# Optimization experiments

Measured on AMD Instinct MI355X. Metric: run time of the kernel, lower is better.

The kernel has to match this reference:

```python
import jax, jax.numpy as jnp
import numpy as np
from jax import lax

TEMPERATURE = 34.0
PAD = 1

def setup_inputs() -> dict:
    key = jax.random.key(0)
    ks = jax.random.split(key, 6)
    B, C, H, W = 16, 256, 64, 64
    K, O, kk, hidden = 4, 256, 3, int(256 * 0.25) + 1
    return {
        "x": jax.random.normal(ks[0], (B, C, H, W), jnp.float32),
        "w_fc1": jax.random.normal(ks[1], (hidden, C), jnp.float32) * 0.05,
        "w_fc2": jax.random.normal(ks[2], (K, hidden), jnp.float32) * 0.05,
        "b_fc2": jax.random.normal(ks[3], (K,), jnp.float32) * 0.05,
        "weight": jax.random.normal(ks[4], (K, O, C, kk, kk), jnp.float32) * 0.05,
        "bias": jax.random.normal(ks[5], (K, O), jnp.float32) * 0.05,
    }

def reference(x, w_fc1, w_fc2, b_fc2, weight, bias):
    # attention2d: global avg pool -> 1x1 conv -> relu -> 1x1 conv -> softmax(logits/T)
    pooled = jnp.mean(x, axis=(2, 3))                       # [B, C]
    h = jax.nn.relu(pooled @ w_fc1.T)                       # [B, hidden]
    logits = h @ w_fc2.T + b_fc2                            # [B, K]
    att = jax.nn.softmax(logits / TEMPERATURE, axis=1)      # [B, K]

    K = weight.shape[0]
    # per-sample aggregated kernels/bias
    agg_w = jnp.einsum('bk,koihw->boihw', att, weight)      # [B, O, C, k, k]
    agg_b = att @ bias                                      # [B, O]

    def conv_one(xi, wi):
        # xi: [C, H, W], wi: [O, C, k, k]
        return lax.conv_general_dilated(
            xi[None], wi, window_strides=(1, 1),
            padding=[(PAD, PAD), (PAD, PAD)],
            dimension_numbers=('NCHW', 'OIHW', 'NCHW'))[0]

    out = jax.vmap(conv_one)(x, agg_w)                      # [B, O, H, W]
    return out + agg_b[:, :, None, None]
```

## Files before the change

### kernel.cpp

```cpp
#include <hip/hip_runtime.h>
#include <math.h>

constexpr int B   = 16;
constexpr int C   = 256;
constexpr int H   = 64;
constexpr int W   = 64;
constexpr int K   = 4;
constexpr int O   = 256;
constexpr int HID = 65;
constexpr float TEMP = 34.0f;

typedef __bf16 bf16x8 __attribute__((ext_vector_type(8)));
typedef float  f32x16 __attribute__((ext_vector_type(16)));
typedef unsigned short ushort_t;

__device__ inline ushort_t f2bf(float f) {
    union { float f; unsigned u; } v; v.f = f;
    unsigned u = v.u;
    u += 0x7FFF + ((u >> 16) & 1);
    return (ushort_t)(u >> 16);
}

__device__ inline void gl2lds16(const void* g, void* l) {
    __builtin_amdgcn_global_load_lds(
        (const __attribute__((address_space(1))) unsigned int*)g,
        (__attribute__((address_space(3))) unsigned int*)l, 16, 0, 0);
}

__global__ void tp_kernel(const float* __restrict__ x,
                          ushort_t* __restrict__ xT,
                          float* __restrict__ pooled) {
    const int ci = blockIdx.x, yg = blockIdx.y, b = blockIdx.z;
    const int tid = threadIdx.x;
    const int cc = tid >> 4;
    const int yy = tid & 15;
    const int y  = yg * 16 + yy;
    const int c  = ci * 16 + cc;

    __shared__ ushort_t t_lds[16 * 1040];
    __shared__ float pool_l[16];
    if (tid < 16) pool_l[tid] = 0.f;
    __syncthreads();

    const float4* src = (const float4*)(x + (((size_t)b * C + c) * H + y) * W);
    float s = 0.f;
    #pragma unroll
    for (int i = 0; i < 16; ++i) {
        float4 v = src[i];
        s += (v.x + v.y) + (v.z + v.w);
        ushort_t* d = &t_lds[yy * 1040 + (4 * i) * 16 + cc];
        d[0]  = f2bf(v.x);
        d[16] = f2bf(v.y);
        d[32] = f2bf(v.z);
        d[48] = f2bf(v.w);
    }
    atomicAdd(&pool_l[cc], s);
    __syncthreads();
    if (tid < 16)
        atomicAdd(&pooled[b * C + ci * 16 + tid], pool_l[tid] * (1.0f / (H * W)));

    const int w    = tid >> 6;
    const int lane = tid & 63;
    const int col  = lane >> 1;
    const int half = lane & 1;
    #pragma unroll
    for (int q = 0; q < 4; ++q) {
        const int y2 = w * 4 + q;
        ushort_t* gbase = xT + ((((size_t)b * 16 + ci) * 64 + (yg * 16 + y2)) * 64) * 16;
        #pragma unroll
        for (int sseg = 0; sseg < 2; ++sseg) {
            uint4 v = *(const uint4*)&t_lds[y2 * 1040 + (sseg * 32 + col) * 16 + half * 8];
            *(uint4*)(gbase + sseg * 512 + lane * 8) = v;
        }
    }
}

__global__ void attention_kernel(const float* __restrict__ pooled,
                                 const float* __restrict__ w_fc1,
                                 const float* __restrict__ w_fc2,
                                 const float* __restrict__ b_fc2,
                                 float* __restrict__ att) {
    const int b = blockIdx.x;
    const int tid = threadIdx.x;
    __shared__ float pool_s[C];
    __shared__ float h_s[HID];
    __shared__ float logit_s[K];

    for (int i = tid; i < C; i += blockDim.x) pool_s[i] = pooled[b * C + i];
    __syncthreads();
    for (int j = tid; j < HID; j += blockDim.x) {
        const float* wr = w_fc1 + (size_t)j * C;
        float s = 0.f;
        #pragma unroll 4
        for (int c = 0; c < C; ++c) s += pool_s[c] * wr[c];
        h_s[j] = fmaxf(s, 0.f);
    }
    __syncthreads();
    if (tid < K) {
        const float* wr = w_fc2 + (size_t)tid * HID;
        float s = b_fc2[tid];
        for (int j = 0; j < HID; ++j) s += h_s[j] * wr[j];
        logit_s[tid] = s * (1.0f / TEMP);
    }
    __syncthreads();
    if (tid == 0) {
        float m = fmaxf(fmaxf(logit_s[0], logit_s[1]), fmaxf(logit_s[2], logit_s[3]));
        float e0 = expf(logit_s[0] - m), e1 = expf(logit_s[1] - m);
        float e2 = expf(logit_s[2] - m), e3 = expf(logit_s[3] - m);
        float inv = 1.0f / (e0 + e1 + e2 + e3);
        att[b * K + 0] = e0 * inv; att[b * K + 1] = e1 * inv;
        att[b * K + 2] = e2 * inv; att[b * K + 3] = e3 * inv;
    }
}

__global__ void wagg_kernel(const float* __restrict__ weight,
                            const float* __restrict__ att,
                            ushort_t* __restrict__ wagg_sw) {
    const int o = blockIdx.x;
    const int tid = threadIdx.x;
    const int oct = tid >> 3;
    const int bg  = tid & 7;

    __shared__ float att_s[B * K];
    if (tid < B * K) att_s[tid] = att[tid];
    __syncthreads();

    const int mi   = o >> 5;
    const int lm   = o & 31;
    const int ci   = oct >> 1;
    const int half = oct & 1;
    const int lane = half * 32 + lm;

    for (int t = 0; t < 9; ++t) {
        float w0[8], w1[8], w2[8], w3[8];
        #pragma unroll
        for (int j = 0; j < 8; ++j) {
            const size_t cidx = (size_t)(oct * 8 + j) * 9 + t;
            w0[j] = weight[((size_t)(0 * O + o) * C) * 9 + cidx];
            w1[j] = weight[((size_t)(1 * O + o) * C) * 9 + cidx];
            w2[j] = weight[((size_t)(2 * O + o) * C) * 9 + cidx];
            w3[j] = weight[((size_t)(3 * O + o) * C) * 9 + cidx];
        }
        #pragma unroll
        for (int bb = 0; bb < 2; ++bb) {
            const int b = bg * 2 + bb;
            const float a0 = att_s[b * K + 0], a1 = att_s[b * K + 1];
            const float a2 = att_s[b * K + 2], a3 = att_s[b * K + 3];
            union { ushort_t u[8]; uint4 v; } pk;
            #pragma unroll
            for (int j = 0; j < 8; ++j)
                pk.u[j] = f2bf(a0 * w0[j] + a1 * w1[j] + a2 * w2[j] + a3 * w3[j]);
            size_t idx = ((((size_t)b * 16 + ci) * 9 + t) * 8 + mi) * 512 + lane * 8;
            *(uint4*)&wagg_sw[idx] = pk.v;
        }
    }
}

__global__ __launch_bounds__(256, 2)
void conv_mfma_kernel(const ushort_t* __restrict__ xT,
                      const ushort_t* __restrict__ wagg_sw,
                      const float* __restrict__ bias,
                      const float* __restrict__ att,
                      float* __restrict__ out) {
    const int b  = blockIdx.x;
    const int yt = blockIdx.y;
    const int oz = blockIdx.z;
    const int y0 = yt * 4;

    const int tid  = threadIdx.x;
    const int lane = tid & 63;
    const int wid  = tid >> 6;
    const int n16  = lane & 31;
    const int khalf = lane >> 5;

    __shared__ __align__(16) ushort_t A_lds[9 * 4 * 512];
    __shared__ __align__(16) ushort_t x_lds[6 * 66 * 16];

    for (int i = tid; i < 6 * 66 * 16; i += 256) x_lds[i] = 0;

    f32x16 acc[4][2];
    #pragma unroll
    for (int a = 0; a < 4; ++a)
        #pragma unroll
        for (int ni = 0; ni < 2; ++ni)
            acc[a][ni] = (f32x16)(0.f);

    for (int ci = 0; ci < 16; ++ci) {
        __syncthreads();

        for (int i = wid; i < 36; i += 4) {
            const int t = i >> 2, a = i & 3;
            const ushort_t* g = wagg_sw
                + ((((size_t)b * 16 + ci) * 9 + t) * 8 + (oz * 4 + a)) * 512 + lane * 8;
            gl2lds16(g, &A_lds[(t * 4 + a) * 512]);
        }
        for (int r = wid; r < 6; r += 4) {
            const int y = y0 - 1 + r;
            if ((unsigned)y < (unsigned)H) {
                const ushort_t* gr = xT + ((((size_t)b * 16 + ci) * 64 + y) * 64) * 16;
                #pragma unroll
                for (int h = 0; h < 2; ++h)
                    gl2lds16(gr + h * 512 + lane * 8,
                             &x_lds[r * (66 * 16) + 16 + h * 512]);
            }
        }

        __syncthreads();

        #pragma unroll
        for (int dy = 0; dy < 3; ++dy) {
            const int r = wid + dy;
            #pragma unroll
            for (int dx = 0; dx < 3; ++dx) {
                const int t = dy * 3 + dx;
                bf16x8 bf[2];
                #pragma unroll
                for (int ni = 0; ni < 2; ++ni)
                    bf[ni] = *(const bf16x8*)&x_lds[r * (66 * 16)
                              + (ni * 32 + n16 + dx) * 16 + khalf * 8];
                #pragma unroll
                for (int a = 0; a < 4; ++a) {
                    bf16x8 af = *(const bf16x8*)&A_lds[(t * 4 + a) * 512 + lane * 8];
                    acc[a][0] = __builtin_amdgcn_mfma_f32_32x32x16_bf16(af, bf[0], acc[a][0], 0, 0, 0);
                    acc[a][1] = __builtin_amdgcn_mfma_f32_32x32x16_bf16(af, bf[1], acc[a][1], 0, 0, 0);
                }
            }
        }
    }

    __syncthreads();
    float* aggb = (float*)A_lds;
    if (tid < 128) {
        const int o = oz * 128 + tid;
        aggb[tid] = att[b * K + 0] * bias[0 * O + o] + att[b * K + 1] * bias[1 * O + o]
                  + att[b * K + 2] * bias[2 * O + o] + att[b * K + 3] * bias[3 * O + o];
    }
    __syncthreads();

    const int y = y0 + wid;
    #pragma unroll
    for (int a = 0; a < 4; ++a) {
        #pragma unroll
        for (int ni = 0; ni < 2; ++ni) {
            #pragma unroll
            for (int reg = 0; reg < 16; ++reg) {
                const int row = (reg & 3) + 8 * (reg >> 2) + 4 * khalf;
                const int ol  = a * 32 + row;
                out[(((size_t)b * O + oz * 128 + ol) * H + y) * W + ni * 32 + n16]
                    = acc[a][ni][reg] + aggb[ol];
            }
        }
    }
}

__global__ void pool_kernel(const float* __restrict__ x, float* __restrict__ pooled) {
    const int bc = blockIdx.x;
    const float4* p4 = (const float4*)(x + (size_t)bc * (H * W));
    const int tid = threadIdx.x;
    float s = 0.f;
    #pragma unroll
    for (int i = 0; i < (H * W / 4) / 256; ++i) {
        float4 v = p4[tid + i * 256];
        s += (v.x + v.y) + (v.z + v.w);
    }
    #pragma unroll
    for (int off = 32; off > 0; off >>= 1) s += __shfl_down(s, off, 64);
    __shared__ float red[4];
    if ((tid & 63) == 0) red[tid >> 6] = s;
    __syncthreads();
    if (tid == 0) pooled[bc] = ((red[0] + red[1]) + (red[2] + red[3])) * (1.0f / (H * W));
}

constexpr int TILE_H = 32;
constexpr int TILE_W = 64;
constexpr int CCF = 4, OT = 8, PX = 8;
constexpr int XS_STRIDE = TILE_W + 3;

__global__ __launch_bounds__(256, 2)
void conv_kernel(const float* __restrict__ x, const float* __restrict__ weight,
                 const float* __restrict__ bias, const float* __restrict__ att,
                 float* __restrict__ out) {
    const int tile_y = blockIdx.x, o0 = blockIdx.y * OT, b = blockIdx.z;
    const int tid = threadIdx.x, tx = tid & 7, ty = tid >> 3, ty0 = tile_y * TILE_H;
    __shared__ __align__(16) float xs[CCF][TILE_H + 2][XS_STRIDE];
    __shared__ __align__(16) float ws_s[OT][CCF][12];
    const float a0 = att[b * K + 0], a1 = att[b * K + 1];
    const float a2 = att[b * K + 2], a3 = att[b * K + 3];
    float acc[OT][PX];
    #pragma unroll
    for (int o = 0; o < OT; ++o)
        #pragma unroll
        for (int p = 0; p < PX; ++p) acc[o][p] = 0.f;
    const float* xb = x + (size_t)b * C * H * W;
    constexpr int X_ELEMS = CCF * (TILE_H + 2) * (TILE_W + 2);
    constexpr int W_ELEMS = OT * CCF * 9;
    for (int c0 = 0; c0 < C; c0 += CCF) {
        __syncthreads();
        for (int idx = tid; idx < X_ELEMS; idx += 256) {
            int cc = idx / ((TILE_H + 2) * (TILE_W + 2));
            int rem = idx - cc * ((TILE_H + 2) * (TILE_W + 2));
            int r = rem / (TILE_W + 2), col = rem - r * (TILE_W + 2);
            int gy = ty0 - 1 + r, gx = col - 1;
            float v = 0.f;
            if ((unsigned)gy < (unsigned)H && (unsigned)gx < (unsigned)W)
                v = xb[((size_t)(c0 + cc) * H + gy) * W + gx];
            xs[cc][r][col] = v;
        }
        for (int idx = tid; idx < W_ELEMS; idx += 256) {
            int o = idx / (CCF * 9), rem = idx - o * (CCF * 9);
            int cc = rem / 9, tap = rem - cc * 9;
            size_t base = ((size_t)(o0 + o) * C + (c0 + cc)) * 9 + tap;
            ws_s[o][cc][tap] = a0 * weight[base] + a1 * weight[(size_t)1 * O * C * 9 + base]
                             + a2 * weight[(size_t)2 * O * C * 9 + base]
                             + a3 * weight[(size_t)3 * O * C * 9 + base];
        }
        __syncthreads();
        #pragma unroll
        for (int cc = 0; cc < CCF; ++cc) {
            float xv[3][10];
            #pragma unroll
            for (int dy = 0; dy < 3; ++dy)
                #pragma unroll
                for (int j = 0; j < 10; ++j) xv[dy][j] = xs[cc][ty + dy][8 * tx + j];
            #pragma unroll
            for (int o = 0; o < OT; ++o) {
                float4 w0 = *(const float4*)&ws_s[o][cc][0];
                float4 w1 = *(const float4*)&ws_s[o][cc][4];
                float w8 = ws_s[o][cc][8];
                #pragma unroll
                for (int p = 0; p < PX; ++p) {
                    float s = acc[o][p];
                    s = fmaf(xv[0][p + 0], w0.x, s); s = fmaf(xv[0][p + 1], w0.y, s);
                    s = fmaf(xv[0][p + 2], w0.z, s); s = fmaf(xv[1][p + 0], w0.w, s);
                    s = fmaf(xv[1][p + 1], w1.x, s); s = fmaf(xv[1][p + 2], w1.y, s);
                    s = fmaf(xv[2][p + 0], w1.z, s); s = fmaf(xv[2][p + 1], w1.w, s);
                    s = fmaf(xv[2][p + 2], w8, s);
                    acc[o][p] = s;
                }
            }
        }
    }
    const int oy = ty0 + ty, ox = 8 * tx;
    #pragma unroll
    for (int o = 0; o < OT; ++o) {
        float ab = a0 * bias[0 * O + o0 + o] + a1 * bias[1 * O + o0 + o]
                 + a2 * bias[2 * O + o0 + o] + a3 * bias[3 * O + o0 + o];
        float4 v0 = make_float4(acc[o][0] + ab, acc[o][1] + ab, acc[o][2] + ab, acc[o][3] + ab);
        float4 v1 = make_float4(acc[o][4] + ab, acc[o][5] + ab, acc[o][6] + ab, acc[o][7] + ab);
        float* op = out + (((size_t)b * O + (o0 + o)) * H + oy) * W + ox;
        *(float4*)(op) = v0; *(float4*)(op + 4) = v1;
    }
}

extern "C" void kernel_launch(void* const* d_in, const int* in_sizes, int n_in,
                              void* d_out, int out_size, void* d_ws, size_t ws_size,
                              hipStream_t stream) {
    const float* x      = (const float*)d_in[0];
    const float* w_fc1  = (const float*)d_in[1];
    const float* w_fc2  = (const float*)d_in[2];
    const float* b_fc2  = (const float*)d_in[3];
    const float* weight = (const float*)d_in[4];
    const float* bias   = (const float*)d_in[5];
    float* out = (float*)d_out;

    float* pooled = (float*)d_ws;
    float* att    = pooled + B * C;
    ushort_t* wagg_sw = (ushort_t*)((char*)d_ws + 32 * 1024);
    const size_t wagg_bytes = (size_t)B * 16 * 9 * 8 * 512 * 2;
    ushort_t* xT = (ushort_t*)((char*)wagg_sw + wagg_bytes);
    const size_t xT_bytes = (size_t)B * 16 * 64 * 64 * 16 * 2;
    const size_t needed = 32 * 1024 + wagg_bytes + xT_bytes;

    if (ws_size >= needed) {
        hipMemsetAsync(pooled, 0, B * C * sizeof(float), stream);
        tp_kernel<<<dim3(16, 4, B), dim3(256), 0, stream>>>(x, xT, pooled);
        attention_kernel<<<dim3(B), dim3(128), 0, stream>>>(pooled, w_fc1, w_fc2, b_fc2, att);
        wagg_kernel<<<dim3(O), dim3(256), 0, stream>>>(weight, att, wagg_sw);
        conv_mfma_kernel<<<dim3(B, 16, 2), dim3(256), 0, stream>>>(xT, wagg_sw, bias, att, out);
    } else {
        pool_kernel<<<dim3(B * C), dim3(256), 0, stream>>>(x, pooled);
        attention_kernel<<<dim3(B), dim3(128), 0, stream>>>(pooled, w_fc1, w_fc2, b_fc2, att);
        conv_kernel<<<dim3(H / TILE_H, O / OT, B), dim3(256), 0, stream>>>(x, weight, bias, att, out);
    }
}
```

Before: 227.9 us.

## Fuse x transpose into conv, register-prefetch A fragments, double-buffer LDS

Removes the separate transpose kernel and its bf16 xT intermediate. The conv kernel now loads fp32 x directly, converts it to bf16 and writes it into a double-buffered LDS tile, prefetching the next channel group into registers while MFMAs run. Weight fragments are read straight from global memory into registers, two taps ahead, instead of being staged through LDS. Pooling returns to a standalone kernel, attention uses float4 loads, and wagg stages its weights through LDS so global reads are coalesced. The trade-off is strided fp32 loads of x (eight channel planes per thread), with each x row re-read by every block that needs it, plus higher register pressure.

```diff
diff --git a/kernel.cpp b/kernel.cpp
--- a/kernel.cpp
+++ b/kernel.cpp
@@ -21,58 +21,22 @@
     return (ushort_t)(u >> 16);
 }
 
-__device__ inline void gl2lds16(const void* g, void* l) {
-    __builtin_amdgcn_global_load_lds(
-        (const __attribute__((address_space(1))) unsigned int*)g,
-        (__attribute__((address_space(3))) unsigned int*)l, 16, 0, 0);
-}
-
-__global__ void tp_kernel(const float* __restrict__ x,
-                          ushort_t* __restrict__ xT,
-                          float* __restrict__ pooled) {
-    const int ci = blockIdx.x, yg = blockIdx.y, b = blockIdx.z;
+__global__ void pool_kernel(const float* __restrict__ x, float* __restrict__ pooled) {
+    const int bc = blockIdx.x;
+    const float4* p4 = (const float4*)(x + (size_t)bc * (H * W));
     const int tid = threadIdx.x;
-    const int cc = tid >> 4;
-    const int yy = tid & 15;
-    const int y  = yg * 16 + yy;
-    const int c  = ci * 16 + cc;
-
-    __shared__ ushort_t t_lds[16 * 1040];
-    __shared__ float pool_l[16];
-    if (tid < 16) pool_l[tid] = 0.f;
-    __syncthreads();
-
-    const float4* src = (const float4*)(x + (((size_t)b * C + c) * H + y) * W);
     float s = 0.f;
     #pragma unroll
-    for (int i = 0; i < 16; ++i) {
-        float4 v = src[i];
+    for (int i = 0; i < (H * W / 4) / 256; ++i) {
+        float4 v = p4[tid + i * 256];
         s += (v.x + v.y) + (v.z + v.w);
-        ushort_t* d = &t_lds[yy * 1040 + (4 * i) * 16 + cc];
-        d[0]  = f2bf(v.x);
-        d[16] = f2bf(v.y);
-        d[32] = f2bf(v.z);
-        d[48] = f2bf(v.w);
-    }
-    atomicAdd(&pool_l[cc], s);
-    __syncthreads();
-    if (tid < 16)
-        atomicAdd(&pooled[b * C + ci * 16 + tid], pool_l[tid] * (1.0f / (H * W)));
-
-    const int w    = tid >> 6;
-    const int lane = tid & 63;
-    const int col  = lane >> 1;
-    const int half = lane & 1;
-    #pragma unroll
-    for (int q = 0; q < 4; ++q) {
-        const int y2 = w * 4 + q;
-        ushort_t* gbase = xT + ((((size_t)b * 16 + ci) * 64 + (yg * 16 + y2)) * 64) * 16;
-        #pragma unroll
-        for (int sseg = 0; sseg < 2; ++sseg) {
-            uint4 v = *(const uint4*)&t_lds[y2 * 1040 + (sseg * 32 + col) * 16 + half * 8];
-            *(uint4*)(gbase + sseg * 512 + lane * 8) = v;
-        }
-    }
+    }
+    #pragma unroll
+    for (int off = 32; off > 0; off >>= 1) s += __shfl_down(s, off, 64);
+    __shared__ float red[4];
+    if ((tid & 63) == 0) red[tid >> 6] = s;
+    __syncthreads();
+    if (tid == 0) pooled[bc] = ((red[0] + red[1]) + (red[2] + red[3])) * (1.0f / (H * W));
 }
 
 __global__ void attention_kernel(const float* __restrict__ pooled,
@@ -86,14 +50,18 @@
     __shared__ float h_s[HID];
     __shared__ float logit_s[K];
 
-    for (int i = tid; i < C; i += blockDim.x) pool_s[i] = pooled[b * C + i];
-    __syncthreads();
-    for (int j = tid; j < HID; j += blockDim.x) {
-        const float* wr = w_fc1 + (size_t)j * C;
+    for (int i = tid; i < C; i += 128) pool_s[i] = pooled[b * C + i];
+    __syncthreads();
+    if (tid < HID) {
+        const float4* wr = (const float4*)(w_fc1 + (size_t)tid * C);
         float s = 0.f;
-        #pragma unroll 4
-        for (int c = 0; c < C; ++c) s += pool_s[c] * wr[c];
-        h_s[j] = fmaxf(s, 0.f);
+        #pragma unroll 8
+        for (int c4 = 0; c4 < C / 4; ++c4) {
+            float4 wv = wr[c4];
+            const float* p = &pool_s[c4 * 4];
+            s += wv.x * p[0] + wv.y * p[1] + wv.z * p[2] + wv.w * p[3];
+        }
+        h_s[tid] = fmaxf(s, 0.f);
     }
     __syncthreads();
     if (tid < K) {
@@ -118,13 +86,21 @@
                             ushort_t* __restrict__ wagg_sw) {
     const int o = blockIdx.x;
     const int tid = threadIdx.x;
+
+    __shared__ float w_lds[4][2304];
+    __shared__ float att_s[B * K];
+
+    #pragma unroll
+    for (int k = 0; k < 4; ++k) {
+        const float4* src = (const float4*)(weight + ((size_t)(k * O + o)) * 2304);
+        for (int i = tid; i < 576; i += 256)
+            ((float4*)w_lds[k])[i] = src[i];
+    }
+    if (tid < B * K) att_s[tid] = att[tid];
+    __syncthreads();
+
     const int oct = tid >> 3;
     const int bg  = tid & 7;
-
-    __shared__ float att_s[B * K];
-    if (tid < B * K) att_s[tid] = att[tid];
-    __syncthreads();
-
     const int mi   = o >> 5;
     const int lm   = o & 31;
     const int ci   = oct >> 1;
@@ -135,29 +111,27 @@
         float w0[8], w1[8], w2[8], w3[8];
         #pragma unroll
         for (int j = 0; j < 8; ++j) {
-            const size_t cidx = (size_t)(oct * 8 + j) * 9 + t;
-            w0[j] = weight[((size_t)(0 * O + o) * C) * 9 + cidx];
-            w1[j] = weight[((size_t)(1 * O + o) * C) * 9 + cidx];
-            w2[j] = weight[((size_t)(2 * O + o) * C) * 9 + cidx];
-            w3[j] = weight[((size_t)(3 * O + o) * C) * 9 + cidx];
+            const int cidx = (oct * 8 + j) * 9 + t;
+            w0[j] = w_lds[0][cidx]; w1[j] = w_lds[1][cidx];
+            w2[j] = w_lds[2][cidx]; w3[j] = w_lds[3][cidx];
         }
         #pragma unroll
         for (int bb = 0; bb < 2; ++bb) {
-            const int b = bg * 2 + bb;
-            const float a0 = att_s[b * K + 0], a1 = att_s[b * K + 1];
-            const float a2 = att_s[b * K + 2], a3 = att_s[b * K + 3];
+            const int bs = bg * 2 + bb;
+            const float a0 = att_s[bs * K + 0], a1 = att_s[bs * K + 1];
+            const float a2 = att_s[bs * K + 2], a3 = att_s[bs * K + 3];
             union { ushort_t u[8]; uint4 v; } pk;
             #pragma unroll
             for (int j = 0; j < 8; ++j)
                 pk.u[j] = f2bf(a0 * w0[j] + a1 * w1[j] + a2 * w2[j] + a3 * w3[j]);
-            size_t idx = ((((size_t)b * 16 + ci) * 9 + t) * 8 + mi) * 512 + lane * 8;
+            size_t idx = ((((size_t)bs * 16 + ci) * 9 + t) * 8 + mi) * 512 + lane * 8;
             *(uint4*)&wagg_sw[idx] = pk.v;
         }
     }
 }
 
 __global__ __launch_bounds__(256, 2)
-void conv_mfma_kernel(const ushort_t* __restrict__ xT,
+void conv_mfma_kernel(const float* __restrict__ x,
                       const ushort_t* __restrict__ wagg_sw,
                       const float* __restrict__ bias,
                       const float* __restrict__ att,
@@ -173,10 +147,16 @@
     const int n16  = lane & 31;
     const int khalf = lane >> 5;
 
-    __shared__ __align__(16) ushort_t A_lds[9 * 4 * 512];
-    __shared__ __align__(16) ushort_t x_lds[6 * 66 * 16];
-
-    for (int i = tid; i < 6 * 66 * 16; i += 256) x_lds[i] = 0;
+    __shared__ __align__(16) ushort_t x_lds[2][6 * 1056];
+
+    for (int i = tid; i < 2 * 6336; i += 256) ((ushort_t*)x_lds)[i] = 0;
+
+    const int scol = lane;
+    const int soct = wid & 1;
+    const int srh  = wid >> 1;
+
+    const uint4* A_base = (const uint4*)wagg_sw
+        + (size_t)b * 73728 + (size_t)oz * 256 + lane;
 
     f32x16 acc[4][2];
     #pragma unroll
@@ -185,51 +165,81 @@
         for (int ni = 0; ni < 2; ++ni)
             acc[a][ni] = (f32x16)(0.f);
 
-    for (int ci = 0; ci < 16; ++ci) {
-        __syncthreads();
-
-        for (int i = wid; i < 36; i += 4) {
-            const int t = i >> 2, a = i & 3;
-            const ushort_t* g = wagg_sw
-                + ((((size_t)b * 16 + ci) * 9 + t) * 8 + (oz * 4 + a)) * 512 + lane * 8;
-            gl2lds16(g, &A_lds[(t * 4 + a) * 512]);
-        }
-        for (int r = wid; r < 6; r += 4) {
+    float xv[3][8];
+    auto gload = [&](int ci) {
+        #pragma unroll
+        for (int rr = 0; rr < 3; ++rr) {
+            const int y = y0 - 1 + srh * 3 + rr;
+            if ((unsigned)y < (unsigned)H) {
+                const float* src = x + (((size_t)b * C + ci * 16 + soct * 8) * H + y) * W + scol;
+                #pragma unroll
+                for (int j = 0; j < 8; ++j)
+                    xv[rr][j] = src[(size_t)j * H * W];
+            }
+        }
+    };
+    auto xwrite = [&](int buf) {
+        #pragma unroll
+        for (int rr = 0; rr < 3; ++rr) {
+            const int r = srh * 3 + rr;
             const int y = y0 - 1 + r;
             if ((unsigned)y < (unsigned)H) {
-                const ushort_t* gr = xT + ((((size_t)b * 16 + ci) * 64 + y) * 64) * 16;
+                union { ushort_t u[8]; uint4 v; } pk;
                 #pragma unroll
-                for (int h = 0; h < 2; ++h)
-                    gl2lds16(gr + h * 512 + lane * 8,
-                             &x_lds[r * (66 * 16) + 16 + h * 512]);
+                for (int j = 0; j < 8; ++j) pk.u[j] = f2bf(xv[rr][j]);
+                *(uint4*)&x_lds[buf][r * 1056 + (scol + 1) * 16 + soct * 8] = pk.v;
             }
         }
-
+    };
+
+    uint4 aE[4], aO[4];
+    auto aload = [&](uint4 (&sl)[4], int s) {
+        const uint4* g = A_base + (size_t)s * 512;
+        #pragma unroll
+        for (int a = 0; a < 4; ++a) sl[a] = g[a * 64];
+    };
+    auto tap = [&](uint4 (&sl)[4], int buf, int t, int s) {
+        const int dy = t / 3, dx = t % 3;
+        const int r = wid + dy;
+        bf16x8 b0 = *(const bf16x8*)&x_lds[buf][r * 1056 + (n16 + dx) * 16 + khalf * 8];
+        bf16x8 b1 = *(const bf16x8*)&x_lds[buf][r * 1056 + (32 + n16 + dx) * 16 + khalf * 8];
+        #pragma unroll
+        for (int a = 0; a < 4; ++a) {
+            bf16x8 af = *(const bf16x8*)&sl[a];
+            acc[a][0] = __builtin_amdgcn_mfma_f32_32x32x16_bf16(af, b0, acc[a][0], 0, 0, 0);
+            acc[a][1] = __builtin_amdgcn_mfma_f32_32x32x16_bf16(af, b1, acc[a][1], 0, 0, 0);
+        }
+        if (s + 2 < 144) aload(sl, s + 2);
+    };
+
+    aload(aE, 0);
+    aload(aO, 1);
+    gload(0);
+    __syncthreads();
+    xwrite(0);
+    __syncthreads();
+
+    for (int cc = 0; cc < 8; ++cc) {
+        const int ci0 = cc * 2;
+        gload(ci0 + 1);
+        #pragma unroll
+        for (int t = 0; t < 9; ++t) {
+            const int s = ci0 * 9 + t;
+            if (t & 1) tap(aO, 0, t, s); else tap(aE, 0, t, s);
+        }
+        xwrite(1);
         __syncthreads();
-
-        #pragma unroll
-        for (int dy = 0; dy < 3; ++dy) {
-            const int r = wid + dy;
-            #pragma unroll
-            for (int dx = 0; dx < 3; ++dx) {
-                const int t = dy * 3 + dx;
-                bf16x8 bf[2];
-                #pragma unroll
-                for (int ni = 0; ni < 2; ++ni)
-                    bf[ni] = *(const bf16x8*)&x_lds[r * (66 * 16)
-                              + (ni * 32 + n16 + dx) * 16 + khalf * 8];
-                #pragma unroll
-                for (int a = 0; a < 4; ++a) {
-                    bf16x8 af = *(const bf16x8*)&A_lds[(t * 4 + a) * 512 + lane * 8];
-                    acc[a][0] = __builtin_amdgcn_mfma_f32_32x32x16_bf16(af, bf[0], acc[a][0], 0, 0, 0);
-                    acc[a][1] = __builtin_amdgcn_mfma_f32_32x32x16_bf16(af, bf[1], acc[a][1], 0, 0, 0);
-                }
-            }
-        }
-    }
-
-    __syncthreads();
-    float* aggb = (float*)A_lds;
+        if (ci0 + 2 < 16) gload(ci0 + 2);
+        #pragma unroll
+        for (int t = 0; t < 9; ++t) {
+            const int s = (ci0 + 1) * 9 + t;
+            if (t & 1) tap(aE, 1, t, s); else tap(aO, 1, t, s);
+        }
+        if (ci0 + 2 < 16) xwrite(0);
+        __syncthreads();
+    }
+
+    float* aggb = (float*)x_lds;
     if (tid < 128) {
         const int o = oz * 128 + tid;
         aggb[tid] = att[b * K + 0] * bias[0 * O + o] + att[b * K + 1] * bias[1 * O + o]
@@ -251,24 +261,6 @@
             }
         }
     }
-}
-
-__global__ void pool_kernel(const float* __restrict__ x, float* __restrict__ pooled) {
-    const int bc = blockIdx.x;
-    const float4* p4 = (const float4*)(x + (size_t)bc * (H * W));
-    const int tid = threadIdx.x;
-    float s = 0.f;
-    #pragma unroll
-    for (int i = 0; i < (H * W / 4) / 256; ++i) {
-        float4 v = p4[tid + i * 256];
-        s += (v.x + v.y) + (v.z + v.w);
-    }
-    #pragma unroll
-    for (int off = 32; off > 0; off >>= 1) s += __shfl_down(s, off, 64);
-    __shared__ float red[4];
-    if ((tid & 63) == 0) red[tid >> 6] = s;
-    __syncthreads();
-    if (tid == 0) pooled[bc] = ((red[0] + red[1]) + (red[2] + red[3])) * (1.0f / (H * W));
 }
 
 constexpr int TILE_H = 32;
@@ -367,19 +359,15 @@
     float* att    = pooled + B * C;
     ushort_t* wagg_sw = (ushort_t*)((char*)d_ws + 32 * 1024);
     const size_t wagg_bytes = (size_t)B * 16 * 9 * 8 * 512 * 2;
-    ushort_t* xT = (ushort_t*)((char*)wagg_sw + wagg_bytes);
-    const size_t xT_bytes = (size_t)B * 16 * 64 * 64 * 16 * 2;
-    const size_t needed = 32 * 1024 + wagg_bytes + xT_bytes;
+    const size_t needed = 32 * 1024 + wagg_bytes;
+
+    pool_kernel<<<dim3(B * C), dim3(256), 0, stream>>>(x, pooled);
+    attention_kernel<<<dim3(B), dim3(128), 0, stream>>>(pooled, w_fc1, w_fc2, b_fc2, att);
 
     if (ws_size >= needed) {
-        hipMemsetAsync(pooled, 0, B * C * sizeof(float), stream);
-        tp_kernel<<<dim3(16, 4, B), dim3(256), 0, stream>>>(x, xT, pooled);
-        attention_kernel<<<dim3(B), dim3(128), 0, stream>>>(pooled, w_fc1, w_fc2, b_fc2, att);
         wagg_kernel<<<dim3(O), dim3(256), 0, stream>>>(weight, att, wagg_sw);
-        conv_mfma_kernel<<<dim3(B, 16, 2), dim3(256), 0, stream>>>(xT, wagg_sw, bias, att, out);
+        conv_mfma_kernel<<<dim3(B, 16, 2), dim3(256), 0, stream>>>(x, wagg_sw, bias, att, out);
     } else {
-        pool_kernel<<<dim3(B * C), dim3(256), 0, stream>>>(x, pooled);
-        attention_kernel<<<dim3(B), dim3(128), 0, stream>>>(pooled, w_fc1, w_fc2, b_fc2, att);
         conv_kernel<<<dim3(H / TILE_H, O / OT, B), dim3(256), 0, stream>>>(x, weight, bias, att, out);
     }
 }
```

New measurement: 236.7 us. 1.04x slower.
